# Kernel tuning notes

Measured on AMD Instinct MI355X. Metric: run time of the kernel, lower is better.

The kernel has to match this reference:

```python
import jax, jax.numpy as jnp
import numpy as np
import math

B, L, D, H, TOPK = 2, 2048, 1024, 16, 5
DK = D // H
U = min(TOPK * int(np.ceil(np.log1p(L))), L)  # = 40 selected queries


def setup_inputs() -> dict:
    k = jax.random.key(0)
    ks = jax.random.split(k, 9)
    s = 1.0 / math.sqrt(D)  # ~ torch Linear init scale
    return {
        "query": jax.random.normal(ks[0], (B, L, D), jnp.float32),
        "key": jax.random.normal(ks[1], (B, L, D), jnp.float32),
        "value": jax.random.normal(ks[2], (B, L, D), jnp.float32),
        "Wq": jax.random.uniform(ks[3], (D, D), jnp.float32, -s, s),
        "bq": jax.random.uniform(ks[4], (D,), jnp.float32, -s, s),
        "Wk": jax.random.uniform(ks[5], (D, D), jnp.float32, -s, s),
        "bk": jax.random.uniform(ks[6], (D,), jnp.float32, -s, s),
        "Wv": jax.random.uniform(ks[7], (D, D), jnp.float32, -s, s),
        "bv": jax.random.uniform(ks[8], (D,), jnp.float32, -s, s),
    }


def reference(query, key, value, Wq, bq, Wk, bk, Wv, bv):
    # torch Linear: y = x @ W.T + b ; split_heads -> [B, H, L, DK]
    def split(x):
        return x.reshape(B, L, H, DK).transpose(0, 2, 1, 3)

    Q = split(query @ Wq.T + bq)
    K = split(key @ Wk.T + bk)
    V = split(value @ Wv.T + bv)

    # Full score matrix [B,H,L,L]; used only for the sparsity measure M
    # (original's Q_K_sample actually uses full K; sampling is dead code).
    scores_full = jnp.einsum('bhqd,bhkd->bhqk', Q, K)
    M = scores_full.max(axis=-1) - scores_full.mean(axis=-1)  # [B,H,L]

    _, M_top = jax.lax.top_k(M, U)  # [B,H,U] (torch uses sorted=False; set identical)

    Q_red = jnp.take_along_axis(Q, M_top[..., None], axis=2)  # [B,H,U,DK]
    attn_scores = jnp.einsum('bhqd,bhkd->bhqk', Q_red, K) / math.sqrt(DK)

    # default causal mask rows gathered at the selected query positions
    causal = jnp.triu(jnp.ones((L, L), jnp.float32), 1)  # [L_Q, L_K]
    attn_scores = attn_scores + causal[M_top] * (-1e9)   # [B,H,U,L]

    attn_probs = jax.nn.softmax(attn_scores, axis=-1)
    attn = jnp.einsum('bhql,bhld->bqhd', attn_probs, V).reshape(B, U, D)
    return attn, attn_probs
```

## Files before the change

kernel.cpp:

```cpp
#include <hip/hip_runtime.h>
#include <hip/hip_bf16.h>

#define BB 2
#define LL 2048
#define DD 1024
#define HH 16
#define DK 64
#define UU 40
#define BH (BB*HH)

typedef unsigned short u16;
typedef float f32x4 __attribute__((ext_vector_type(4)));
typedef short s16x8 __attribute__((ext_vector_type(8)));

__device__ inline float b2f_r8(u16 x) {
    union { unsigned short u; __hip_bfloat16 b; } c; c.u = x;
    return __bfloat162float(c.b);
}
__device__ inline float ldf_r8(const void* p, size_t i, int isF) {
    return isF ? ((const float*)p)[i] : b2f_r8(((const u16*)p)[i]);
}
__device__ inline f32x4 ld4_r8(const void* p, size_t i, int isF) {
    if (isF) return *(const f32x4*)((const float*)p + i);
    ushort4 v = *(const ushort4*)((const u16*)p + i);
    f32x4 r;
    r[0] = b2f_r8(v.x); r[1] = b2f_r8(v.y); r[2] = b2f_r8(v.z); r[3] = b2f_r8(v.w);
    return r;
}
__device__ inline void cvt2_r8(float x, u16& h, u16& l) {
    union { __hip_bfloat16 b; u16 u; } ch, cl;
    ch.b = __float2bfloat16(x);
    float hf = __bfloat162float(ch.b);
    cl.b = __float2bfloat16(x - hf);
    h = ch.u; l = cl.u;
}

__global__ __launch_bounds__(256) void detect_dtype_r8(const u16* __restrict__ q,
                                                       int* __restrict__ flag) {
    __shared__ float red[256];
    int tid = threadIdx.x;
    float mx = 0.f;
    for (int i = tid; i < 4096; i += 256) {
        float v = fabsf(b2f_r8(q[i]));
        if (!(v < 1e30f)) v = 1e38f;
        mx = fmaxf(mx, v);
    }
    red[tid] = mx; __syncthreads();
    for (int s = 128; s > 0; s >>= 1) {
        if (tid < s) red[tid] = fmaxf(red[tid], red[tid + s]);
        __syncthreads();
    }
    if (tid == 0) *flag = (red[0] > 1e20f) ? 1 : 0;
}

#define PAD 132

__global__ __launch_bounds__(256) void proj_f4_r11(
    const void* __restrict__ key, const void* __restrict__ query,
    const void* __restrict__ Wk, const void* __restrict__ Wq,
    const void* __restrict__ bk, const void* __restrict__ bq,
    float* __restrict__ Kf, float* __restrict__ Qf,
    const int* __restrict__ flag)
{
    __shared__ float sX[64 * PAD];
    __shared__ float sW[64 * PAD];
    int tid = threadIdx.x;
    int n0 = blockIdx.x * 128, f0 = blockIdx.y * 128, z = blockIdx.z;
    const void* X    = z ? query : key;
    const void* W    = z ? Wq    : Wk;
    const void* bias = z ? bq    : bk;
    float* out       = z ? Qf    : Kf;
    int isF = *flag;
    int tx = tid & 15, ty = tid >> 4;

    float acc[8][8];
#pragma unroll
    for (int a = 0; a < 8; ++a)
#pragma unroll
        for (int c = 0; c < 8; ++c) acc[a][c] = 0.f;

    for (int kc = 0; kc < 16; ++kc) {
        __syncthreads();
#pragma unroll
        for (int it = 0; it < 8; ++it) {
            int row = 64 * (it & 1) + (tid >> 2);
            int d4 = (tid & 3) | ((it >> 1) << 2);
            f32x4 v = ld4_r8(X, (size_t)(n0 + row) * DD + kc * 64 + d4 * 4, isF);
#pragma unroll
            for (int cc = 0; cc < 4; ++cc)
                sX[(4 * d4 + cc) * PAD + row] = v[cc];
        }
#pragma unroll
        for (int it = 0; it < 8; ++it) {
            int row = 64 * (it & 1) + (tid >> 2);
            int d4 = (tid & 3) | ((it >> 1) << 2);
            f32x4 v = ld4_r8(W, (size_t)(f0 + row) * DD + kc * 64 + d4 * 4, isF);
#pragma unroll
            for (int cc = 0; cc < 4; ++cc)
                sW[(4 * d4 + cc) * PAD + row] = v[cc];
        }
        __syncthreads();
        for (int d = 0; d < 64; ++d) {
            const f32x4 xa = *(const f32x4*)(&sX[d * PAD + ty * 4]);
            const f32x4 xb = *(const f32x4*)(&sX[d * PAD + 64 + ty * 4]);
            const f32x4 wa = *(const f32x4*)(&sW[d * PAD + tx * 4]);
            const f32x4 wb = *(const f32x4*)(&sW[d * PAD + 64 + tx * 4]);
            float xv[8] = {xa[0], xa[1], xa[2], xa[3], xb[0], xb[1], xb[2], xb[3]};
            float wv[8] = {wa[0], wa[1], wa[2], wa[3], wb[0], wb[1], wb[2], wb[3]};
#pragma unroll
            for (int a = 0; a < 8; ++a)
#pragma unroll
                for (int c = 0; c < 8; ++c)
                    acc[a][c] = fmaf(xv[a], wv[c], acc[a][c]);
        }
    }
#pragma unroll
    for (int a = 0; a < 8; ++a) {
        int n = n0 + (a >> 2) * 64 + ty * 4 + (a & 3);
        int b = n >> 11, l = n & (LL - 1);
#pragma unroll
        for (int c = 0; c < 8; ++c) {
            int f = f0 + (c >> 2) * 64 + tx * 4 + (c & 3);
            int h = f >> 6, dk = f & 63;
            out[((size_t)(b * HH + h) * LL + l) * DK + dk] =
                acc[a][c] + ldf_r8(bias, (size_t)f, isF);
        }
    }
}

#define LDK 72
__global__ __launch_bounds__(256) void proj_mfma_v_r9(
    const void* __restrict__ X, const void* __restrict__ W,
    const void* __restrict__ bias, float* __restrict__ out,
    const int* __restrict__ flag)
{
    __shared__ u16 Ahi[128 * LDK];
    __shared__ u16 Alo[128 * LDK];
    __shared__ u16 Bhi[128 * LDK];
    __shared__ u16 Blo[128 * LDK];
    int tid = threadIdx.x;
    int n0 = blockIdx.x * 128, f0 = blockIdx.y * 128;
    int isF = *flag;
    int lane = tid & 63, w = tid >> 6, wr = w >> 1, wc = w & 1;

    f32x4 acc[4][4] = {};

    for (int kc = 0; kc < 16; ++kc) {
        __syncthreads();
#pragma unroll
        for (int it = 0; it < 16; ++it) {
            int i = it * 256 + tid;
            int isB = i >> 11, j = i & 2047;
            int row = j >> 4, c = (j & 15) << 2;
            f32x4 v = ld4_r8(isB ? W : X, (size_t)((isB ? f0 : n0) + row) * DD + kc * 64 + c, isF);
            u16* hh = isB ? Bhi : Ahi;
            u16* ll = isB ? Blo : Alo;
            ushort4 h4, l4;
            cvt2_r8(v[0], h4.x, l4.x);
            cvt2_r8(v[1], h4.y, l4.y);
            cvt2_r8(v[2], h4.z, l4.z);
            cvt2_r8(v[3], h4.w, l4.w);
            *(ushort4*)&hh[row * LDK + c] = h4;
            *(ushort4*)&ll[row * LDK + c] = l4;
        }
        __syncthreads();
#pragma unroll
        for (int kk = 0; kk < 2; ++kk) {
            int koff = kk * 32 + (lane >> 4) * 8;
            s16x8 ah[4], al[4];
#pragma unroll
            for (int mi = 0; mi < 4; ++mi) {
                int r = wr * 64 + mi * 16 + (lane & 15);
                ah[mi] = *(const s16x8*)&Ahi[r * LDK + koff];
                al[mi] = *(const s16x8*)&Alo[r * LDK + koff];
            }
#pragma unroll
            for (int ni = 0; ni < 4; ++ni) {
                int r = wc * 64 + ni * 16 + (lane & 15);
                s16x8 bh = *(const s16x8*)&Bhi[r * LDK + koff];
                s16x8 bl = *(const s16x8*)&Blo[r * LDK + koff];
#pragma unroll
                for (int mi = 0; mi < 4; ++mi) {
                    acc[mi][ni] = __builtin_amdgcn_mfma_f32_16x16x32_bf16(ah[mi], bh, acc[mi][ni], 0, 0, 0);
                    acc[mi][ni] = __builtin_amdgcn_mfma_f32_16x16x32_bf16(al[mi], bh, acc[mi][ni], 0, 0, 0);
                    acc[mi][ni] = __builtin_amdgcn_mfma_f32_16x16x32_bf16(ah[mi], bl, acc[mi][ni], 0, 0, 0);
                }
            }
        }
    }

#pragma unroll
    for (int ni = 0; ni < 4; ++ni) {
        int f = f0 + wc * 64 + ni * 16 + (lane & 15);
        float bb = ldf_r8(bias, (size_t)f, isF);
        int h = f >> 6, dk = f & 63;
#pragma unroll
        for (int mi = 0; mi < 4; ++mi) {
            int nbase = n0 + wr * 64 + mi * 16 + ((lane >> 4) << 2);
#pragma unroll
            for (int j2 = 0; j2 < 4; ++j2) {
                int n = nbase + j2, b = n >> 11, l = n & (LL - 1);
                out[((size_t)(b * HH + h) * LL + l) * DK + dk] = acc[mi][ni][j2] + bb;
            }
        }
    }
}

__global__ __launch_bounds__(256) void kbar_r8(
    const float* __restrict__ Kf, double* __restrict__ Kbar)
{
    __shared__ double red[256];
    int bh = blockIdx.x, tid = threadIdx.x;
    int d = tid & 63, seg = tid >> 6;
    double s = 0;
    for (int l = seg * 512; l < seg * 512 + 512; ++l)
        s += (double)Kf[((size_t)bh * LL + l) * DK + d];
    red[tid] = s; __syncthreads();
    if (tid < 128) red[tid] += red[tid + 128];
    __syncthreads();
    if (tid < 64) Kbar[(size_t)bh * DK + d] = (red[tid] + red[tid + 64]) * (1.0 / (double)LL);
}

#define QT 128
#define KT 128
__global__ __launch_bounds__(256) void stats_max_r10(
    const float* __restrict__ Qf, const float* __restrict__ Kf,
    const double* __restrict__ Kbar, double* __restrict__ Mv)
{
    __shared__ float sQ[64 * PAD];
    __shared__ float sK[64 * PAD];
    __shared__ float rowmax[QT];
    int tid = threadIdx.x;
    int q0 = blockIdx.x * QT, bh = blockIdx.y;
    int tx = tid & 15, ty = tid >> 4;

    {
        const float* src = Qf + ((size_t)bh * LL + q0) * DK;
#pragma unroll
        for (int it = 0; it < 8; ++it) {
            int row = 64 * (it & 1) + (tid >> 2);
            int d4 = (tid & 3) | ((it >> 1) << 2);
            f32x4 v = *(const f32x4*)(src + (size_t)row * DK + d4 * 4);
#pragma unroll
            for (int cc = 0; cc < 4; ++cc)
                sQ[(4 * d4 + cc) * PAD + row] = v[cc];
        }
    }
    float rmax8[8];
#pragma unroll
    for (int a = 0; a < 8; ++a) rmax8[a] = -INFINITY;

    const float* kbase = Kf + (size_t)bh * LL * DK;
    for (int kc = 0; kc < LL / KT; ++kc) {
        __syncthreads();
#pragma unroll
        for (int it = 0; it < 8; ++it) {
            int row = 64 * (it & 1) + (tid >> 2);
            int d4 = (tid & 3) | ((it >> 1) << 2);
            f32x4 v = *(const f32x4*)(kbase + (size_t)(kc * KT + row) * DK + d4 * 4);
#pragma unroll
            for (int cc = 0; cc < 4; ++cc)
                sK[(4 * d4 + cc) * PAD + row] = v[cc];
        }
        __syncthreads();
        float acc[8][8];
#pragma unroll
        for (int a = 0; a < 8; ++a)
#pragma unroll
            for (int c = 0; c < 8; ++c) acc[a][c] = 0.f;
        for (int d = 0; d < 64; ++d) {
            const f32x4 qa = *(const f32x4*)(&sQ[d * PAD + ty * 4]);
            const f32x4 qb = *(const f32x4*)(&sQ[d * PAD + 64 + ty * 4]);
            const f32x4 ka = *(const f32x4*)(&sK[d * PAD + tx * 4]);
            const f32x4 kb = *(const f32x4*)(&sK[d * PAD + 64 + tx * 4]);
            float qv[8] = {qa[0], qa[1], qa[2], qa[3], qb[0], qb[1], qb[2], qb[3]};
            float kv[8] = {ka[0], ka[1], ka[2], ka[3], kb[0], kb[1], kb[2], kb[3]};
#pragma unroll
            for (int a = 0; a < 8; ++a)
#pragma unroll
                for (int c = 0; c < 8; ++c)
                    acc[a][c] = fmaf(qv[a], kv[c], acc[a][c]);
        }
#pragma unroll
        for (int a = 0; a < 8; ++a)
#pragma unroll
            for (int c = 0; c < 8; ++c) rmax8[a] = fmaxf(rmax8[a], acc[a][c]);
    }
#pragma unroll
    for (int a = 0; a < 8; ++a) {
        float v = rmax8[a];
        v = fmaxf(v, __shfl_xor(v, 1));
        v = fmaxf(v, __shfl_xor(v, 2));
        v = fmaxf(v, __shfl_xor(v, 4));
        v = fmaxf(v, __shfl_xor(v, 8));
        rmax8[a] = v;
    }
    if (tx == 0) {
#pragma unroll
        for (int a = 0; a < 8; ++a) {
            int row = ty * 4 + (a & 3) + (a >> 2) * 64;
            rowmax[row] = rmax8[a];
        }
    }
    __syncthreads();
    if (tid < QT) {
        const double* kb = Kbar + (size_t)bh * DK;
        double s = 0;
#pragma unroll
        for (int d = 0; d < 64; ++d) s += (double)sQ[d * PAD + tid] * kb[d];
        Mv[(size_t)bh * LL + q0 + tid] = (double)rowmax[tid] - s;
    }
}

__global__ __launch_bounds__(64) void topk_wave_r10(
    const double* __restrict__ Mv, int* __restrict__ sel)
{
    int bh = blockIdx.x, lane = threadIdx.x;
    double v[32];
#pragma unroll
    for (int t = 0; t < 32; ++t) v[t] = Mv[(size_t)bh * LL + t * 64 + lane];
    for (int u = 0; u < UU; ++u) {
        double bv = -1e301; int bi = LL;
#pragma unroll
        for (int t = 0; t < 32; ++t) {
            double x = v[t]; int j = t * 64 + lane;
            if (x > bv || (x == bv && j < bi)) { bv = x; bi = j; }
        }
#pragma unroll
        for (int off = 1; off < 64; off <<= 1) {
            double ov = __shfl_xor(bv, off); int oi = __shfl_xor(bi, off);
            if (ov > bv || (ov == bv && oi < bi)) { bv = ov; bi = oi; }
        }
        if ((bi & 63) == lane) {
            int ts = bi >> 6;
#pragma unroll
            for (int t = 0; t < 32; ++t)
                if (t == ts) v[t] = -1e302;
        }
        if (lane == 0) sel[bh * UU + u] = bi;
    }
}

__global__ __launch_bounds__(256) void attn_out4_r11(
    const float* __restrict__ Qf, const float* __restrict__ Kf,
    const float* __restrict__ Vf, const int* __restrict__ sel,
    float* __restrict__ attnOut, float* __restrict__ probsOut)
{
    __shared__ float qs[DK];
    __shared__ float pl[LL];
    __shared__ float red[256];
    __shared__ f32x4 sred4[16 * 16];
    int id = blockIdx.x;
    int xcd = id & 7, t = id >> 3;
    int u = t % 40, bh = ((t / 40) << 3) | xcd;
    int tid = threadIdx.x;
    int b = bh >> 4, h = bh & 15;
    int qpos = sel[bh * UU + u];

    if (tid < DK) qs[tid] = Qf[((size_t)bh * LL + qpos) * DK + tid];
    __syncthreads();

    f32x4 qv[16];
#pragma unroll
    for (int i = 0; i < 16; ++i) qv[i] = *(const f32x4*)(&qs[i * 4]);

    const float* kb = Kf + (size_t)bh * LL * DK;
    float sloc[8];
    float lmax = -INFINITY;
#pragma unroll
    for (int c = 0; c < 8; ++c) {
        int l = c * 256 + tid;
        const f32x4* kr = (const f32x4*)(kb + (size_t)l * DK);
        float s = 0.f;
#pragma unroll
        for (int i = 0; i < 16; ++i) {
            const f32x4 kvv = kr[i];
            s = fmaf(qv[i][0], kvv[0], s);
            s = fmaf(qv[i][1], kvv[1], s);
            s = fmaf(qv[i][2], kvv[2], s);
            s = fmaf(qv[i][3], kvv[3], s);
        }
        s *= 0.125f;
        if (l > qpos) s -= 1e9f;
        sloc[c] = s;
        lmax = fmaxf(lmax, s);
    }
    red[tid] = lmax; __syncthreads();
    for (int s2 = 128; s2 > 0; s2 >>= 1) {
        if (tid < s2) red[tid] = fmaxf(red[tid], red[tid + s2]);
        __syncthreads();
    }
    float mval = red[0];
    __syncthreads();
    float lsum = 0.f;
#pragma unroll
    for (int c = 0; c < 8; ++c) { sloc[c] = expf(sloc[c] - mval); lsum += sloc[c]; }
    red[tid] = lsum; __syncthreads();
    for (int s2 = 128; s2 > 0; s2 >>= 1) {
        if (tid < s2) red[tid] += red[tid + s2];
        __syncthreads();
    }
    float inv = 1.0f / red[0];
    size_t rowo = ((size_t)bh * UU + u) * LL;
#pragma unroll
    for (int c = 0; c < 8; ++c) {
        int l = c * 256 + tid;
        float p = sloc[c] * inv;
        pl[l] = p;
        probsOut[rowo + l] = p;
    }
    __syncthreads();

    int tx = tid & 15, g = tid >> 4;
    int dk4 = tx * 4;
    const float* vb = Vf + (size_t)bh * LL * DK;
    float ax = 0.f, ay = 0.f, az = 0.f, aw = 0.f;
#pragma unroll 4
    for (int l = g * 128; l < g * 128 + 128; ++l) {
        float p = pl[l];
        const f32x4 v = *(const f32x4*)(vb + (size_t)l * DK + dk4);
        ax = fmaf(p, v[0], ax);
        ay = fmaf(p, v[1], ay);
        az = fmaf(p, v[2], az);
        aw = fmaf(p, v[3], aw);
    }
    f32x4 acc4; acc4[0] = ax; acc4[1] = ay; acc4[2] = az; acc4[3] = aw;
    sred4[g * 16 + tx] = acc4;
    __syncthreads();
    if (tid < 64) {
        float s = 0.f;
#pragma unroll
        for (int g2 = 0; g2 < 16; ++g2) {
            const float* sp = (const float*)&sred4[g2 * 16 + (tid >> 2)];
            s += sp[tid & 3];
        }
        attnOut[((size_t)b * UU + u) * DD + h * DK + tid] = s;
    }
}

extern "C" void kernel_launch(void* const* d_in, const int* in_sizes, int n_in,
                              void* d_out, int out_size, void* d_ws, size_t ws_size,
                              hipStream_t stream) {
    (void)in_sizes; (void)n_in; (void)out_size; (void)ws_size;
    const void* query = d_in[0];
    const void* key   = d_in[1];
    const void* value = d_in[2];
    const void* Wq    = d_in[3];
    const void* bq    = d_in[4];
    const void* Wk    = d_in[5];
    const void* bk    = d_in[6];
    const void* Wv    = d_in[7];
    const void* bv    = d_in[8];

    char* w = (char*)d_ws;
    const size_t NE = (size_t)BB * HH * LL * DK;
    float* Kf  = (float*)w;  w += NE * 4;
    float* Vf  = (float*)w;  w += NE * 4;
    float* Qf  = (float*)w;  w += NE * 4;
    double* Mv = (double*)w; w += (size_t)BH * LL * 8;
    double* Kbar = (double*)w; w += (size_t)BH * DK * 8;
    int* sel   = (int*)w;    w += (size_t)BH * UU * 4;
    int* flag  = (int*)w;    w += 64;

    float* attnOut  = (float*)d_out;
    float* probsOut = attnOut + (size_t)BB * UU * DD;

    dim3 blk(256);
    detect_dtype_r8<<<1, blk, 0, stream>>>((const u16*)query, flag);
    proj_f4_r11<<<dim3(32, 8, 2), blk, 0, stream>>>(key, query, Wk, Wq, bk, bq,
                                                    Kf, Qf, flag);
    proj_mfma_v_r9<<<dim3(32, 8), blk, 0, stream>>>(value, Wv, bv, Vf, flag);
    kbar_r8<<<32, blk, 0, stream>>>(Kf, Kbar);
    stats_max_r10<<<dim3(LL / QT, 32), blk, 0, stream>>>(Qf, Kf, Kbar, Mv);
    topk_wave_r10<<<32, dim3(64), 0, stream>>>(Mv, sel);
    attn_out4_r11<<<1280, blk, 0, stream>>>(Qf, Kf, Vf, sel, attnOut, probsOut);
}
```

Before: 999.5 us.

## Split attention into tiled score, softmax and PV kernels; shrink projection and stats tiles

The per-query attention kernel, which re-read the whole K and V of a head for each of the 40 selected queries, is replaced by four kernels. A tiled score kernel shares each K tile across all 40 queries, a separate softmax pass follows, and a PV kernel computes partial sums over 256-key chunks, which a small kernel then reduces. The projection kernel also halves its K-chunk depth, and the stats-max kernel uses a 64-key tile with an 8x4 register block, both cutting LDS use and register pressure to raise occupancy. The cost is extra launches, a scores buffer round-tripped through global memory, and less arithmetic reuse per thread in the stats kernel.

```diff
diff --git a/kernel.cpp b/kernel.cpp
--- a/kernel.cpp
+++ b/kernel.cpp
@@ -55,15 +55,15 @@
 
 #define PAD 132
 
-__global__ __launch_bounds__(256) void proj_f4_r11(
+__global__ __launch_bounds__(256) void proj_f4_r12(
     const void* __restrict__ key, const void* __restrict__ query,
     const void* __restrict__ Wk, const void* __restrict__ Wq,
     const void* __restrict__ bk, const void* __restrict__ bq,
     float* __restrict__ Kf, float* __restrict__ Qf,
     const int* __restrict__ flag)
 {
-    __shared__ float sX[64 * PAD];
-    __shared__ float sW[64 * PAD];
+    __shared__ float sX[32 * PAD];
+    __shared__ float sW[32 * PAD];
     int tid = threadIdx.x;
     int n0 = blockIdx.x * 128, f0 = blockIdx.y * 128, z = blockIdx.z;
     const void* X    = z ? query : key;
@@ -79,28 +79,28 @@
 #pragma unroll
         for (int c = 0; c < 8; ++c) acc[a][c] = 0.f;
 
-    for (int kc = 0; kc < 16; ++kc) {
-        __syncthreads();
-#pragma unroll
-        for (int it = 0; it < 8; ++it) {
-            int row = 64 * (it & 1) + (tid >> 2);
-            int d4 = (tid & 3) | ((it >> 1) << 2);
-            f32x4 v = ld4_r8(X, (size_t)(n0 + row) * DD + kc * 64 + d4 * 4, isF);
+    for (int kc = 0; kc < 32; ++kc) {
+        __syncthreads();
+#pragma unroll
+        for (int it = 0; it < 4; ++it) {
+            int idx = it * 256 + tid;
+            int row = idx >> 3, d4 = idx & 7;
+            f32x4 v = ld4_r8(X, (size_t)(n0 + row) * DD + kc * 32 + d4 * 4, isF);
 #pragma unroll
             for (int cc = 0; cc < 4; ++cc)
                 sX[(4 * d4 + cc) * PAD + row] = v[cc];
         }
 #pragma unroll
-        for (int it = 0; it < 8; ++it) {
-            int row = 64 * (it & 1) + (tid >> 2);
-            int d4 = (tid & 3) | ((it >> 1) << 2);
-            f32x4 v = ld4_r8(W, (size_t)(f0 + row) * DD + kc * 64 + d4 * 4, isF);
+        for (int it = 0; it < 4; ++it) {
+            int idx = it * 256 + tid;
+            int row = idx >> 3, d4 = idx & 7;
+            f32x4 v = ld4_r8(W, (size_t)(f0 + row) * DD + kc * 32 + d4 * 4, isF);
 #pragma unroll
             for (int cc = 0; cc < 4; ++cc)
                 sW[(4 * d4 + cc) * PAD + row] = v[cc];
         }
         __syncthreads();
-        for (int d = 0; d < 64; ++d) {
+        for (int d = 0; d < 32; ++d) {
             const f32x4 xa = *(const f32x4*)(&sX[d * PAD + ty * 4]);
             const f32x4 xb = *(const f32x4*)(&sX[d * PAD + 64 + ty * 4]);
             const f32x4 wa = *(const f32x4*)(&sW[d * PAD + tx * 4]);
@@ -222,13 +222,12 @@
 }
 
 #define QT 128
-#define KT 128
-__global__ __launch_bounds__(256) void stats_max_r10(
+__global__ __launch_bounds__(256) void stats_max_r12(
     const float* __restrict__ Qf, const float* __restrict__ Kf,
     const double* __restrict__ Kbar, double* __restrict__ Mv)
 {
     __shared__ float sQ[64 * PAD];
-    __shared__ float sK[64 * PAD];
+    __shared__ float sK[64 * 68];
     __shared__ float rowmax[QT];
     int tid = threadIdx.x;
     int q0 = blockIdx.x * QT, bh = blockIdx.y;
@@ -251,40 +250,38 @@
     for (int a = 0; a < 8; ++a) rmax8[a] = -INFINITY;
 
     const float* kbase = Kf + (size_t)bh * LL * DK;
-    for (int kc = 0; kc < LL / KT; ++kc) {
-        __syncthreads();
-#pragma unroll
-        for (int it = 0; it < 8; ++it) {
-            int row = 64 * (it & 1) + (tid >> 2);
-            int d4 = (tid & 3) | ((it >> 1) << 2);
-            f32x4 v = *(const f32x4*)(kbase + (size_t)(kc * KT + row) * DK + d4 * 4);
+    for (int kc = 0; kc < 32; ++kc) {
+        __syncthreads();
+#pragma unroll
+        for (int it = 0; it < 4; ++it) {
+            int row = tid >> 2;
+            int d4 = (tid & 3) | (it << 2);
+            f32x4 v = *(const f32x4*)(kbase + (size_t)(kc * 64 + row) * DK + d4 * 4);
 #pragma unroll
             for (int cc = 0; cc < 4; ++cc)
-                sK[(4 * d4 + cc) * PAD + row] = v[cc];
-        }
-        __syncthreads();
-        float acc[8][8];
+                sK[(4 * d4 + cc) * 68 + row] = v[cc];
+        }
+        __syncthreads();
+        float acc[8][4];
 #pragma unroll
         for (int a = 0; a < 8; ++a)
 #pragma unroll
-            for (int c = 0; c < 8; ++c) acc[a][c] = 0.f;
+            for (int c = 0; c < 4; ++c) acc[a][c] = 0.f;
         for (int d = 0; d < 64; ++d) {
             const f32x4 qa = *(const f32x4*)(&sQ[d * PAD + ty * 4]);
             const f32x4 qb = *(const f32x4*)(&sQ[d * PAD + 64 + ty * 4]);
-            const f32x4 ka = *(const f32x4*)(&sK[d * PAD + tx * 4]);
-            const f32x4 kb = *(const f32x4*)(&sK[d * PAD + 64 + tx * 4]);
+            const f32x4 ka = *(const f32x4*)(&sK[d * 68 + tx * 4]);
             float qv[8] = {qa[0], qa[1], qa[2], qa[3], qb[0], qb[1], qb[2], qb[3]};
-            float kv[8] = {ka[0], ka[1], ka[2], ka[3], kb[0], kb[1], kb[2], kb[3]};
 #pragma unroll
             for (int a = 0; a < 8; ++a)
 #pragma unroll
-                for (int c = 0; c < 8; ++c)
-                    acc[a][c] = fmaf(qv[a], kv[c], acc[a][c]);
+                for (int c = 0; c < 4; ++c)
+                    acc[a][c] = fmaf(qv[a], ka[c], acc[a][c]);
         }
 #pragma unroll
         for (int a = 0; a < 8; ++a)
 #pragma unroll
-            for (int c = 0; c < 8; ++c) rmax8[a] = fmaxf(rmax8[a], acc[a][c]);
+            for (int c = 0; c < 4; ++c) rmax8[a] = fmaxf(rmax8[a], acc[a][c]);
     }
 #pragma unroll
     for (int a = 0; a < 8; ++a) {
@@ -341,49 +338,78 @@
     }
 }
 
-__global__ __launch_bounds__(256) void attn_out4_r11(
+__global__ __launch_bounds__(256) void scores_r12(
     const float* __restrict__ Qf, const float* __restrict__ Kf,
-    const float* __restrict__ Vf, const int* __restrict__ sel,
-    float* __restrict__ attnOut, float* __restrict__ probsOut)
-{
-    __shared__ float qs[DK];
-    __shared__ float pl[LL];
+    const int* __restrict__ sel, float* __restrict__ S)
+{
+    __shared__ float sK[256 * 68];
+    __shared__ float qsm[40 * 68];
+    __shared__ int qpos[UU];
+    int lq = blockIdx.x, bh = blockIdx.y, tid = threadIdx.x;
+    int l0 = lq * 256;
+    if (tid < UU) qpos[tid] = sel[bh * UU + tid];
+    __syncthreads();
+    for (int i = tid; i < 640; i += 256) {
+        int u = i >> 4, c4 = i & 15;
+        *(f32x4*)&qsm[u * 68 + c4 * 4] =
+            *(const f32x4*)&Qf[((size_t)bh * LL + qpos[u]) * DK + c4 * 4];
+    }
+#pragma unroll
+    for (int it = 0; it < 16; ++it) {
+        int idx = it * 256 + tid;
+        int l = idx >> 4, d4 = idx & 15;
+        *(f32x4*)&sK[l * 68 + d4 * 4] =
+            *(const f32x4*)&Kf[((size_t)bh * LL + l0 + l) * DK + d4 * 4];
+    }
+    __syncthreads();
+    int gu = tid >> 5, lt = tid & 31;
+    float acc[5][8];
+#pragma unroll
+    for (int ui = 0; ui < 5; ++ui)
+#pragma unroll
+        for (int li = 0; li < 8; ++li) acc[ui][li] = 0.f;
+    for (int d16 = 0; d16 < 16; ++d16) {
+        f32x4 qf[5], kf[8];
+#pragma unroll
+        for (int ui = 0; ui < 5; ++ui)
+            qf[ui] = *(const f32x4*)&qsm[(gu + 8 * ui) * 68 + d16 * 4];
+#pragma unroll
+        for (int li = 0; li < 8; ++li)
+            kf[li] = *(const f32x4*)&sK[(lt + 32 * li) * 68 + d16 * 4];
+#pragma unroll
+        for (int ui = 0; ui < 5; ++ui)
+#pragma unroll
+            for (int li = 0; li < 8; ++li)
+#pragma unroll
+                for (int c = 0; c < 4; ++c)
+                    acc[ui][li] = fmaf(qf[ui][c], kf[li][c], acc[ui][li]);
+    }
+#pragma unroll
+    for (int ui = 0; ui < 5; ++ui) {
+        int u = gu + 8 * ui;
+        int qp = qpos[u];
+#pragma unroll
+        for (int li = 0; li < 8; ++li) {
+            int l = l0 + lt + 32 * li;
+            float s = acc[ui][li] * 0.125f;
+            if (l > qp) s -= 1e9f;
+            S[((size_t)bh * UU + u) * LL + l] = s;
+        }
+    }
+}
+
+__global__ __launch_bounds__(256) void softmax_r12(
+    const float* __restrict__ S, float* __restrict__ probsOut)
+{
     __shared__ float red[256];
-    __shared__ f32x4 sred4[16 * 16];
-    int id = blockIdx.x;
-    int xcd = id & 7, t = id >> 3;
-    int u = t % 40, bh = ((t / 40) << 3) | xcd;
-    int tid = threadIdx.x;
-    int b = bh >> 4, h = bh & 15;
-    int qpos = sel[bh * UU + u];
-
-    if (tid < DK) qs[tid] = Qf[((size_t)bh * LL + qpos) * DK + tid];
-    __syncthreads();
-
-    f32x4 qv[16];
-#pragma unroll
-    for (int i = 0; i < 16; ++i) qv[i] = *(const f32x4*)(&qs[i * 4]);
-
-    const float* kb = Kf + (size_t)bh * LL * DK;
+    int u = blockIdx.x, bh = blockIdx.y, tid = threadIdx.x;
+    size_t rowo = ((size_t)bh * UU + u) * LL;
     float sloc[8];
     float lmax = -INFINITY;
 #pragma unroll
     for (int c = 0; c < 8; ++c) {
-        int l = c * 256 + tid;
-        const f32x4* kr = (const f32x4*)(kb + (size_t)l * DK);
-        float s = 0.f;
-#pragma unroll
-        for (int i = 0; i < 16; ++i) {
-            const f32x4 kvv = kr[i];
-            s = fmaf(qv[i][0], kvv[0], s);
-            s = fmaf(qv[i][1], kvv[1], s);
-            s = fmaf(qv[i][2], kvv[2], s);
-            s = fmaf(qv[i][3], kvv[3], s);
-        }
-        s *= 0.125f;
-        if (l > qpos) s -= 1e9f;
-        sloc[c] = s;
-        lmax = fmaxf(lmax, s);
+        sloc[c] = S[rowo + c * 256 + tid];
+        lmax = fmaxf(lmax, sloc[c]);
     }
     red[tid] = lmax; __syncthreads();
     for (int s2 = 128; s2 > 0; s2 >>= 1) {
@@ -401,41 +427,69 @@
         __syncthreads();
     }
     float inv = 1.0f / red[0];
-    size_t rowo = ((size_t)bh * UU + u) * LL;
-#pragma unroll
-    for (int c = 0; c < 8; ++c) {
-        int l = c * 256 + tid;
-        float p = sloc[c] * inv;
-        pl[l] = p;
-        probsOut[rowo + l] = p;
+#pragma unroll
+    for (int c = 0; c < 8; ++c)
+        probsOut[rowo + c * 256 + tid] = sloc[c] * inv;
+}
+
+#define PVP 260
+__global__ __launch_bounds__(256) void pv_r12(
+    const float* __restrict__ probsOut, const float* __restrict__ Vf,
+    float* __restrict__ part)
+{
+    __shared__ float sVd[64 * PVP];
+    __shared__ float pP[40 * 256];
+    int lq = blockIdx.x, bh = blockIdx.y, tid = threadIdx.x;
+    int l0 = lq * 256;
+#pragma unroll
+    for (int it = 0; it < 10; ++it) {
+        int idx = it * 256 + tid;
+        int u = idx >> 6, l4 = idx & 63;
+        *(f32x4*)&pP[u * 256 + l4 * 4] =
+            *(const f32x4*)&probsOut[((size_t)bh * UU + u) * LL + l0 + l4 * 4];
+    }
+#pragma unroll
+    for (int it = 0; it < 16; ++it) {
+        int idx = it * 256 + tid;
+        int l = idx >> 4, d4 = idx & 15;
+        f32x4 v = *(const f32x4*)&Vf[((size_t)bh * LL + l0 + l) * DK + d4 * 4];
+#pragma unroll
+        for (int cc = 0; cc < 4; ++cc)
+            sVd[(4 * d4 + cc) * PVP + l] = v[cc];
     }
     __syncthreads();
-
-    int tx = tid & 15, g = tid >> 4;
-    int dk4 = tx * 4;
-    const float* vb = Vf + (size_t)bh * LL * DK;
-    float ax = 0.f, ay = 0.f, az = 0.f, aw = 0.f;
-#pragma unroll 4
-    for (int l = g * 128; l < g * 128 + 128; ++l) {
-        float p = pl[l];
-        const f32x4 v = *(const f32x4*)(vb + (size_t)l * DK + dk4);
-        ax = fmaf(p, v[0], ax);
-        ay = fmaf(p, v[1], ay);
-        az = fmaf(p, v[2], az);
-        aw = fmaf(p, v[3], aw);
-    }
-    f32x4 acc4; acc4[0] = ax; acc4[1] = ay; acc4[2] = az; acc4[3] = aw;
-    sred4[g * 16 + tx] = acc4;
-    __syncthreads();
-    if (tid < 64) {
-        float s = 0.f;
-#pragma unroll
-        for (int g2 = 0; g2 < 16; ++g2) {
-            const float* sp = (const float*)&sred4[g2 * 16 + (tid >> 2)];
-            s += sp[tid & 3];
-        }
-        attnOut[((size_t)b * UU + u) * DD + h * DK + tid] = s;
-    }
+    int dk = tid & 63, ug = tid >> 6;
+    float acc[10];
+#pragma unroll
+    for (int j = 0; j < 10; ++j) acc[j] = 0.f;
+    for (int l4 = 0; l4 < 64; ++l4) {
+        const f32x4 v4 = *(const f32x4*)&sVd[dk * PVP + l4 * 4];
+#pragma unroll
+        for (int j = 0; j < 10; ++j) {
+            const f32x4 p4 = *(const f32x4*)&pP[(ug * 10 + j) * 256 + l4 * 4];
+            acc[j] = fmaf(p4[0], v4[0], acc[j]);
+            acc[j] = fmaf(p4[1], v4[1], acc[j]);
+            acc[j] = fmaf(p4[2], v4[2], acc[j]);
+            acc[j] = fmaf(p4[3], v4[3], acc[j]);
+        }
+    }
+#pragma unroll
+    for (int j = 0; j < 10; ++j) {
+        int u = ug * 10 + j;
+        part[(((size_t)bh * 8 + lq) * UU + u) * DK + dk] = acc[j];
+    }
+}
+
+__global__ __launch_bounds__(64) void pvred_r12(
+    const float* __restrict__ part, float* __restrict__ attnOut)
+{
+    int u = blockIdx.x, bh = blockIdx.y, dk = threadIdx.x;
+    int b = bh >> 4, h = bh & 15;
+    float s = 0.f;
+#pragma unroll
+    for (int lq = 0; lq < 8; ++lq)
+        s += part[(((size_t)bh * 8 + lq) * UU + u) * DK + dk];
+    attnOut[((size_t)b * UU + u) * DD + h * DK + dk] = s;
 }
 
 extern "C" void kernel_launch(void* const* d_in, const int* in_sizes, int n_in,
@@ -461,17 +515,22 @@
     double* Kbar = (double*)w; w += (size_t)BH * DK * 8;
     int* sel   = (int*)w;    w += (size_t)BH * UU * 4;
     int* flag  = (int*)w;    w += 64;
+    float* S    = (float*)w; w += (size_t)BH * UU * LL * 4;
+    float* part = (float*)w; w += (size_t)BH * 8 * UU * DK * 4;
 
     float* attnOut  = (float*)d_out;
     float* probsOut = attnOut + (size_t)BB * UU * DD;
 
     dim3 blk(256);
     detect_dtype_r8<<<1, blk, 0, stream>>>((const u16*)query, flag);
-    proj_f4_r11<<<dim3(32, 8, 2), blk, 0, stream>>>(key, query, Wk, Wq, bk, bq,
+    proj_f4_r12<<<dim3(32, 8, 2), blk, 0, stream>>>(key, query, Wk, Wq, bk, bq,
                                                     Kf, Qf, flag);
     proj_mfma_v_r9<<<dim3(32, 8), blk, 0, stream>>>(value, Wv, bv, Vf, flag);
     kbar_r8<<<32, blk, 0, stream>>>(Kf, Kbar);
-    stats_max_r10<<<dim3(LL / QT, 32), blk, 0, stream>>>(Qf, Kf, Kbar, Mv);
+    stats_max_r12<<<dim3(LL / QT, 32), blk, 0, stream>>>(Qf, Kf, Kbar, Mv);
     topk_wave_r10<<<32, dim3(64), 0, stream>>>(Mv, sel);
-    attn_out4_r11<<<1280, blk, 0, stream>>>(Qf, Kf, Vf, sel, attnOut, probsOut);
-}
+    scores_r12<<<dim3(8, 32), blk, 0, stream>>>(Qf, Kf, sel, S);
+    softmax_r12<<<dim3(UU, 32), blk, 0, stream>>>(S, probsOut);
+    pv_r12<<<dim3(8, 32), blk, 0, stream>>>(probsOut, Vf, part);
+    pvred_r12<<<dim3(UU, 32), dim3(64), 0, stream>>>(part, attnOut);
+}
```

New measurement: 924.0 us. 1.08x faster.
